# Performance work log

Hardware: AMD Instinct MI355X
Metric: run time of the kernel (lower is better)

## Reference

```python
import jax, jax.numpy as jnp
import numpy as np

N_BITS = 3        # routing dims (slice_mask = first 3 indices)
N_HEADS = 8       # 2**N_BITS
D_FEAT = 512      # input_dim - N_BITS
D_BASE = 1024     # base MLP output
D_HEAD_H = 1024   # head hidden
D_OUT = 512       # head output
BATCH = 8192


def setup_inputs() -> dict:
    key = jax.random.key(0)
    ks = jax.random.split(key, 8)
    s = lambda fan_in: 1.0 / np.sqrt(fan_in)
    x = jax.random.normal(ks[0], (BATCH, N_BITS + D_FEAT), dtype=jnp.float32)
    Wb = jax.random.normal(ks[1], (D_FEAT, D_BASE), dtype=jnp.float32) * s(D_FEAT)
    bb = jax.random.normal(ks[2], (D_BASE,), dtype=jnp.float32) * s(D_FEAT)
    Wh1 = jax.random.normal(ks[3], (N_HEADS, D_BASE, D_HEAD_H), dtype=jnp.float32) * s(D_BASE)
    bh1 = jax.random.normal(ks[4], (N_HEADS, D_HEAD_H), dtype=jnp.float32) * s(D_BASE)
    Wh2 = jax.random.normal(ks[5], (N_HEADS, D_HEAD_H, D_OUT), dtype=jnp.float32) * s(D_HEAD_H)
    bh2 = jax.random.normal(ks[6], (N_HEADS, D_OUT), dtype=jnp.float32) * s(D_HEAD_H)
    return {"x": x, "Wb": Wb, "bb": bb, "Wh1": Wh1, "bh1": bh1, "Wh2": Wh2, "bh2": bh2}


def _combs():
    # Faithful to the torch `recursive` construction for three single-index
    # binary slices: combs[bit, head] = (head >> bit) & 1
    return ((jnp.arange(N_HEADS)[None, :] >> jnp.arange(N_BITS)[:, None]) & 1).astype(bool)


def reference(x, Wb, bb, Wh1, bh1, Wh2, bh2):
    bits = x[:, :N_BITS] > 0.5          # [B, 3] routing bits
    feat = x[:, N_BITS:]                # [B, 512]
    base = jax.nn.relu(feat @ Wb + bb)  # [B, 1024] shared base net
    # all heads run over the full batch (as in the original module)
    h = jax.nn.relu(jnp.einsum('bd,hde->bhe', base, Wh1) + bh1[None])  # [B, 8, 1024]
    out_all = jnp.einsum('bhe,heo->bho', h, Wh2) + bh2[None]           # [B, 8, 512]
    combs = _combs()                                                   # [3, 8]
    sel = jnp.all(bits[:, :, None] == combs[None], axis=1).astype(x.dtype)  # [B, 8] one-hot
    return jnp.einsum('bho,bh->bo', out_all, sel)                      # [B, 512]
```

## Files before the change

kernel.cpp:

```cpp
#include <hip/hip_runtime.h>
#include <hip/hip_bf16.h>
#include <stdint.h>

using short8 = __attribute__((ext_vector_type(8))) short;
using f32x4  = __attribute__((ext_vector_type(4))) float;

#define NBITS 3
#define NHEADS 8
#define BATCH 8192
#define DFEAT 512
#define DBASE 1024
#define DHH   1024
#define DOUT  512
#define XCOLS (NBITS + DFEAT)

static __device__ __forceinline__ unsigned short f2bf(float f) {
    union { float f; unsigned u; } v; v.f = f;
    unsigned r = v.u + 0x7FFFu + ((v.u >> 16) & 1u);
    return (unsigned short)(r >> 16);
}

__global__ void k_bucket(const float* __restrict__ x, int* __restrict__ cnt,
                         int* __restrict__ rows) {
    int r = blockIdx.x * 256 + threadIdx.x;
    if (r >= BATCH) return;
    const float* xr = x + (size_t)r * XCOLS;
    int h = (xr[0] > 0.5f ? 1 : 0) | (xr[1] > 0.5f ? 2 : 0) | (xr[2] > 0.5f ? 4 : 0);
    int slot = atomicAdd(cnt + h, 1);
    rows[h * BATCH + slot] = r;
}

__global__ void k_feat(const float* __restrict__ x, unsigned short* __restrict__ feat) {
    int t = blockIdx.x * 256 + threadIdx.x;
    int row = t >> 6, c8 = (t & 63) << 3;
    const float* src = x + (size_t)row * XCOLS + NBITS + c8;
    short8 v;
#pragma unroll
    for (int i = 0; i < 8; ++i) v[i] = (short)f2bf(src[i]);
    *(short8*)(feat + (size_t)row * DFEAT + c8) = v;
}

__global__ void k_transpose(const float* __restrict__ W, unsigned short* __restrict__ WT,
                            int K, int N) {
    __shared__ float tile[32][33];
    int b  = blockIdx.z;
    int n0 = blockIdx.x << 5, k0 = blockIdx.y << 5;
    int tx = threadIdx.x & 31, ty = threadIdx.x >> 5;
    const float* Wb = W + (size_t)b * K * N;
    unsigned short* WTb = WT + (size_t)b * K * N;
#pragma unroll
    for (int j = 0; j < 32; j += 8)
        tile[ty + j][tx] = Wb[(size_t)(k0 + ty + j) * N + n0 + tx];
    __syncthreads();
#pragma unroll
    for (int j = 0; j < 32; j += 8)
        WTb[(size_t)(n0 + ty + j) * K + k0 + tx] = f2bf(tile[tx][ty + j]);
}

template<bool GATHER, bool RELU, bool OUTBF16>
__global__ __launch_bounds__(256, 2)
void k_gemm(const unsigned short* __restrict__ A, int lda, int K,
            const unsigned short* __restrict__ BT,
            const float* __restrict__ bias,
            void* __restrict__ C, int ldc,
            const int* __restrict__ rowsAll, const int* __restrict__ cntAll,
            int Nfull) {
    const int head = blockIdx.z;
    const int m0 = blockIdx.x * 128;
    const int n0 = blockIdx.y * 128;
    int M = BATCH;
    const int* rows = nullptr;
    if (GATHER) {
        M = cntAll[head];
        if (m0 >= M) return;
        rows = rowsAll + head * BATCH;
    }
    const unsigned short* BTh = BT + (size_t)head * Nfull * K;
    const float* biash = bias + (size_t)head * Nfull;

    __shared__ __align__(16) unsigned short As[128 * 32];
    __shared__ __align__(16) unsigned short Bs[128 * 32];

    const int t    = threadIdx.x;
    const int wave = t >> 6;
    const int lane = t & 63;
    const int wr = wave >> 1, wc = wave & 1;

    const unsigned short* gA[2];
    const unsigned short* gB[2];
#pragma unroll
    for (int p = 0; p < 2; ++p) {
        int i = p * 256 + t;
        int idx = m0 + (i >> 2);
        int r;
        if (GATHER) { if (idx >= M) idx = M - 1; r = rows[idx]; }
        else r = idx;
        gA[p] = A + (size_t)r * lda + (i & 3) * 8;
        int nrow = n0 + (i >> 2);
        gB[p] = BTh + (size_t)nrow * K + (i & 3) * 8;
    }
    char* lAs = (char*)As;
    char* lBs = (char*)Bs;

    f32x4 acc[4][4] = {};
    const int ln = lane & 15, lq = lane >> 4;

    for (int kt = 0; kt < K; kt += 32) {
#pragma unroll
        for (int p = 0; p < 2; ++p) {
            __builtin_amdgcn_global_load_lds(
                (const __attribute__((address_space(1))) void*)(gA[p] + kt),
                (__attribute__((address_space(3))) void*)(lAs + (p * 256 + wave * 64) * 16),
                16, 0, 0);
            __builtin_amdgcn_global_load_lds(
                (const __attribute__((address_space(1))) void*)(gB[p] + kt),
                (__attribute__((address_space(3))) void*)(lBs + (p * 256 + wave * 64) * 16),
                16, 0, 0);
        }
        __syncthreads();
        short8 af[4], bfr[4];
#pragma unroll
        for (int m = 0; m < 4; ++m)
            af[m] = *(const short8*)(As + (wr * 64 + m * 16 + ln) * 32 + lq * 8);
#pragma unroll
        for (int n = 0; n < 4; ++n)
            bfr[n] = *(const short8*)(Bs + (wc * 64 + n * 16 + ln) * 32 + lq * 8);
#pragma unroll
        for (int m = 0; m < 4; ++m)
#pragma unroll
            for (int n = 0; n < 4; ++n)
                acc[m][n] = __builtin_amdgcn_mfma_f32_16x16x32_bf16(af[m], bfr[n], acc[m][n], 0, 0, 0);
        __syncthreads();
    }

#pragma unroll
    for (int n = 0; n < 4; ++n) {
        int col = n0 + wc * 64 + n * 16 + ln;
        float bv = biash[col];
#pragma unroll
        for (int m = 0; m < 4; ++m) {
#pragma unroll
            for (int r = 0; r < 4; ++r) {
                int lr = wr * 64 + m * 16 + lq * 4 + r;
                int grow;
                if (GATHER) {
                    if (m0 + lr >= M) continue;
                    grow = rows[m0 + lr];
                } else {
                    grow = m0 + lr;
                }
                float v = acc[m][n][r] + bv;
                if (RELU) v = fmaxf(v, 0.0f);
                if (OUTBF16)
                    ((unsigned short*)C)[(size_t)grow * ldc + col] = f2bf(v);
                else
                    ((float*)C)[(size_t)grow * ldc + col] = v;
            }
        }
    }
}

extern "C" void kernel_launch(void* const* d_in, const int* in_sizes, int n_in,
                              void* d_out, int out_size, void* d_ws, size_t ws_size,
                              hipStream_t stream) {
    const float* x   = (const float*)d_in[0];
    const float* Wb  = (const float*)d_in[1];
    const float* bb  = (const float*)d_in[2];
    const float* Wh1 = (const float*)d_in[3];
    const float* bh1 = (const float*)d_in[4];
    const float* Wh2 = (const float*)d_in[5];
    const float* bh2 = (const float*)d_in[6];

    char* ws = (char*)d_ws;
    unsigned short* feat = (unsigned short*)(ws);
    unsigned short* WbT  = (unsigned short*)(ws + (8ull  << 20));
    unsigned short* Wh1T = (unsigned short*)(ws + (9ull  << 20));
    unsigned short* Wh2T = (unsigned short*)(ws + (25ull << 20));
    unsigned short* base = (unsigned short*)(ws + (33ull << 20));
    unsigned short* hbuf = (unsigned short*)(ws + (49ull << 20));
    int* rows            = (int*)(ws + (65ull << 20));
    int* cnt             = (int*)(ws + (65ull << 20) + (256ull << 10));

    hipMemsetAsync(cnt, 0, NHEADS * sizeof(int), stream);
    k_bucket<<<BATCH / 256, 256, 0, stream>>>(x, cnt, rows);
    k_feat<<<(BATCH * 64) / 256, 256, 0, stream>>>(x, feat);
    k_transpose<<<dim3(DBASE / 32, DFEAT / 32, 1), 256, 0, stream>>>(Wb, WbT, DFEAT, DBASE);
    k_transpose<<<dim3(DHH / 32, DBASE / 32, NHEADS), 256, 0, stream>>>(Wh1, Wh1T, DBASE, DHH);
    k_transpose<<<dim3(DOUT / 32, DHH / 32, NHEADS), 256, 0, stream>>>(Wh2, Wh2T, DHH, DOUT);

    k_gemm<false, true, true><<<dim3(64, DBASE / 128, 1), 256, 0, stream>>>(
        feat, DFEAT, DFEAT, WbT, bb, base, DBASE, nullptr, nullptr, DBASE);
    k_gemm<true, true, true><<<dim3(64, DHH / 128, NHEADS), 256, 0, stream>>>(
        base, DBASE, DBASE, Wh1T, bh1, hbuf, DHH, rows, cnt, DHH);
    k_gemm<true, false, false><<<dim3(64, DOUT / 128, NHEADS), 256, 0, stream>>>(
        hbuf, DHH, DHH, Wh2T, bh2, d_out, DOUT, rows, cnt, DOUT);
}
```

Baseline: 328.7 us.

## Double-buffer LDS tiles in GEMM to overlap global loads with MFMA

```diff
diff --git a/kernel.cpp b/kernel.cpp
--- a/kernel.cpp
+++ b/kernel.cpp
@@ -78,8 +78,8 @@
     const unsigned short* BTh = BT + (size_t)head * Nfull * K;
     const float* biash = bias + (size_t)head * Nfull;
 
-    __shared__ __align__(16) unsigned short As[128 * 32];
-    __shared__ __align__(16) unsigned short Bs[128 * 32];
+    __shared__ __align__(16) unsigned short As[2][128 * 32];
+    __shared__ __align__(16) unsigned short Bs[2][128 * 32];
 
     const int t    = threadIdx.x;
     const int wave = t >> 6;
@@ -101,37 +101,50 @@
     }
     char* lAs = (char*)As;
     char* lBs = (char*)Bs;
+    const int dstOff = (wave * 64) * 16;
+
+#define STAGE(koff, buf)                                                              \
+    {                                                                                 \
+        _Pragma("unroll")                                                             \
+        for (int p = 0; p < 2; ++p) {                                                 \
+            __builtin_amdgcn_global_load_lds(                                         \
+                (const __attribute__((address_space(1))) void*)(gA[p] + (koff)),      \
+                (__attribute__((address_space(3))) void*)(lAs + (buf) * 8192 + p * 4096 + dstOff), \
+                16, 0, 0);                                                            \
+            __builtin_amdgcn_global_load_lds(                                         \
+                (const __attribute__((address_space(1))) void*)(gB[p] + (koff)),      \
+                (__attribute__((address_space(3))) void*)(lBs + (buf) * 8192 + p * 4096 + dstOff), \
+                16, 0, 0);                                                            \
+        }                                                                             \
+    }
 
     f32x4 acc[4][4] = {};
     const int ln = lane & 15, lq = lane >> 4;
-
-    for (int kt = 0; kt < K; kt += 32) {
-#pragma unroll
-        for (int p = 0; p < 2; ++p) {
-            __builtin_amdgcn_global_load_lds(
-                (const __attribute__((address_space(1))) void*)(gA[p] + kt),
-                (__attribute__((address_space(3))) void*)(lAs + (p * 256 + wave * 64) * 16),
-                16, 0, 0);
-            __builtin_amdgcn_global_load_lds(
-                (const __attribute__((address_space(1))) void*)(gB[p] + kt),
-                (__attribute__((address_space(3))) void*)(lBs + (p * 256 + wave * 64) * 16),
-                16, 0, 0);
-        }
-        __syncthreads();
+    const int nt = K >> 5;
+
+    STAGE(0, 0);
+    __syncthreads();
+
+    for (int tk = 0; tk < nt; ++tk) {
+        const int cur = tk & 1;
+        if (tk + 1 < nt) STAGE((tk + 1) << 5, cur ^ 1);
+
         short8 af[4], bfr[4];
 #pragma unroll
         for (int m = 0; m < 4; ++m)
-            af[m] = *(const short8*)(As + (wr * 64 + m * 16 + ln) * 32 + lq * 8);
+            af[m] = *(const short8*)(As[cur] + (wr * 64 + m * 16 + ln) * 32 + lq * 8);
 #pragma unroll
         for (int n = 0; n < 4; ++n)
-            bfr[n] = *(const short8*)(Bs + (wc * 64 + n * 16 + ln) * 32 + lq * 8);
+            bfr[n] = *(const short8*)(Bs[cur] + (wc * 64 + n * 16 + ln) * 32 + lq * 8);
 #pragma unroll
         for (int m = 0; m < 4; ++m)
 #pragma unroll
             for (int n = 0; n < 4; ++n)
                 acc[m][n] = __builtin_amdgcn_mfma_f32_16x16x32_bf16(af[m], bfr[n], acc[m][n], 0, 0, 0);
+
         __syncthreads();
     }
+#undef STAGE
 
 #pragma unroll
     for (int n = 0; n < 4; ++n) {
```

Result: no change. 327.0 us (-0.5%).

## Rewrite GEMM with 128x256 tiles, double-buffered swizzled LDS and software pipelining

Applied to the files above, without the earlier changes.

```diff
diff --git a/kernel.cpp b/kernel.cpp
--- a/kernel.cpp
+++ b/kernel.cpp
@@ -58,16 +58,19 @@
 }
 
 template<bool GATHER, bool RELU, bool OUTBF16>
-__global__ __launch_bounds__(256, 2)
-void k_gemm(const unsigned short* __restrict__ A, int lda, int K,
-            const unsigned short* __restrict__ BT,
-            const float* __restrict__ bias,
-            void* __restrict__ C, int ldc,
-            const int* __restrict__ rowsAll, const int* __restrict__ cntAll,
-            int Nfull) {
-    const int head = blockIdx.z;
-    const int m0 = blockIdx.x * 128;
-    const int n0 = blockIdx.y * 128;
+__global__ __launch_bounds__(512, 1)
+void k_gemm2(const unsigned short* __restrict__ A, int lda, int K,
+             const unsigned short* __restrict__ BT,
+             const float* __restrict__ bias,
+             void* __restrict__ C, int ldc,
+             const int* __restrict__ rowsAll, const int* __restrict__ cntAll,
+             int Nfull, int nshift) {
+    const int bid  = blockIdx.x;
+    const int mt   = bid & 63;
+    const int nt   = (bid >> 6) & ((1 << nshift) - 1);
+    const int head = GATHER ? (bid >> (6 + nshift)) : 0;
+    const int m0 = mt * 128;
+    const int n0 = nt * 256;
     int M = BATCH;
     const int* rows = nullptr;
     if (GATHER) {
@@ -78,60 +81,95 @@
     const unsigned short* BTh = BT + (size_t)head * Nfull * K;
     const float* biash = bias + (size_t)head * Nfull;
 
-    __shared__ __align__(16) unsigned short As[128 * 32];
-    __shared__ __align__(16) unsigned short Bs[128 * 32];
+    __shared__ __align__(16) char lds[98304];
+    char* ldsp = lds;
 
     const int t    = threadIdx.x;
-    const int wave = t >> 6;
+    const int w    = t >> 6;
     const int lane = t & 63;
-    const int wr = wave >> 1, wc = wave & 1;
+    const int wr = w >> 2, wc = w & 3;
+    const int ln = lane & 15, lq = lane >> 4;
 
     const unsigned short* gA[2];
-    const unsigned short* gB[2];
-#pragma unroll
-    for (int p = 0; p < 2; ++p) {
-        int i = p * 256 + t;
-        int idx = m0 + (i >> 2);
-        int r;
-        if (GATHER) { if (idx >= M) idx = M - 1; r = rows[idx]; }
-        else r = idx;
-        gA[p] = A + (size_t)r * lda + (i & 3) * 8;
-        int nrow = n0 + (i >> 2);
-        gB[p] = BTh + (size_t)nrow * K + (i & 3) * 8;
-    }
-    char* lAs = (char*)As;
-    char* lBs = (char*)Bs;
+    {
+        int rl  = t >> 3;
+        int kch = (t & 7) ^ (rl & 7);
+#pragma unroll
+        for (int h = 0; h < 2; ++h) {
+            int idx = m0 + h * 64 + rl;
+            int r;
+            if (GATHER) { idx = idx < M ? idx : (M - 1); r = rows[idx]; }
+            else r = idx;
+            gA[h] = A + (size_t)r * lda + kch * 8;
+        }
+    }
+    const unsigned short* gB[2][2];
+#pragma unroll
+    for (int hb = 0; hb < 2; ++hb)
+#pragma unroll
+        for (int i = 0; i < 2; ++i) {
+            int c   = i * 512 + t;
+            int cl  = c >> 3;
+            int kch = (c & 7) ^ (cl & 7);
+            int ncol = n0 + hb * 128 + cl;
+            gB[hb][i] = BTh + (size_t)ncol * K + kch * 8;
+        }
+
+#define STAGE_A(kt, d)                                                                     \
+    { _Pragma("unroll") for (int h = 0; h < 2; ++h)                                        \
+        __builtin_amdgcn_global_load_lds(                                                  \
+            (const __attribute__((address_space(1))) void*)(gA[h] + (kt) * 64),            \
+            (__attribute__((address_space(3))) void*)(ldsp + (d) * 16384 + h * 8192 + w * 1024), \
+            16, 0, 0); }
+#define STAGE_B(kt, d)                                                                     \
+    { _Pragma("unroll") for (int hb = 0; hb < 2; ++hb)                                     \
+      _Pragma("unroll") for (int i = 0; i < 2; ++i)                                        \
+        __builtin_amdgcn_global_load_lds(                                                  \
+            (const __attribute__((address_space(1))) void*)(gB[hb][i] + (kt) * 64),        \
+            (__attribute__((address_space(3))) void*)(ldsp + 32768 + (d) * 32768 + hb * 16384 + i * 8192 + w * 1024), \
+            16, 0, 0); }
+#define LOAD_A(dst, d, ks)                                                                 \
+    { _Pragma("unroll") for (int m = 0; m < 4; ++m) {                                      \
+        int rA = wr * 64 + m * 16 + ln;                                                    \
+        int ch = (((ks) << 2) | lq) ^ (ln & 7);                                            \
+        dst[m] = *(const short8*)(ldsp + (d) * 16384 + rA * 128 + ch * 16); } }
+#define LOAD_B(dst, d, ks)                                                                 \
+    { _Pragma("unroll") for (int n = 0; n < 4; ++n) {                                      \
+        int cB = wc * 64 + n * 16 + ln;                                                    \
+        int ch = (((ks) << 2) | lq) ^ (ln & 7);                                            \
+        dst[n] = *(const short8*)(ldsp + 32768 + (d) * 32768 + cB * 128 + ch * 16); } }
+#define MFMA16(av, bv)                                                                     \
+    { __builtin_amdgcn_s_setprio(1);                                                       \
+      _Pragma("unroll") for (int m = 0; m < 4; ++m)                                        \
+      _Pragma("unroll") for (int n = 0; n < 4; ++n)                                        \
+        acc[m][n] = __builtin_amdgcn_mfma_f32_16x16x32_bf16(av[m], bv[n], acc[m][n], 0, 0, 0); \
+      __builtin_amdgcn_s_setprio(0); }
 
     f32x4 acc[4][4] = {};
-    const int ln = lane & 15, lq = lane >> 4;
-
-    for (int kt = 0; kt < K; kt += 32) {
-#pragma unroll
-        for (int p = 0; p < 2; ++p) {
-            __builtin_amdgcn_global_load_lds(
-                (const __attribute__((address_space(1))) void*)(gA[p] + kt),
-                (__attribute__((address_space(3))) void*)(lAs + (p * 256 + wave * 64) * 16),
-                16, 0, 0);
-            __builtin_amdgcn_global_load_lds(
-                (const __attribute__((address_space(1))) void*)(gB[p] + kt),
-                (__attribute__((address_space(3))) void*)(lBs + (p * 256 + wave * 64) * 16),
-                16, 0, 0);
-        }
+    short8 a0[4], b0[4], a1[4], b1[4];
+    const int NT = K >> 6;
+
+    STAGE_A(0, 0); STAGE_B(0, 0); STAGE_A(1, 1);
+    __syncthreads();
+    LOAD_A(a0, 0, 0); LOAD_B(b0, 0, 0);
+
+    for (int kt = 0; kt < NT; ++kt) {
+        const int d = kt & 1, o = d ^ 1;
+        const int kB = (kt + 1 < NT) ? kt + 1 : NT - 1;
+        const int kA = (kt + 2 < NT) ? kt + 2 : NT - 1;
+        STAGE_B(kB, o);
+        LOAD_A(a1, d, 1); LOAD_B(b1, d, 1);
+        MFMA16(a0, b0);
         __syncthreads();
-        short8 af[4], bfr[4];
-#pragma unroll
-        for (int m = 0; m < 4; ++m)
-            af[m] = *(const short8*)(As + (wr * 64 + m * 16 + ln) * 32 + lq * 8);
-#pragma unroll
-        for (int n = 0; n < 4; ++n)
-            bfr[n] = *(const short8*)(Bs + (wc * 64 + n * 16 + ln) * 32 + lq * 8);
-#pragma unroll
-        for (int m = 0; m < 4; ++m)
-#pragma unroll
-            for (int n = 0; n < 4; ++n)
-                acc[m][n] = __builtin_amdgcn_mfma_f32_16x16x32_bf16(af[m], bfr[n], acc[m][n], 0, 0, 0);
-        __syncthreads();
-    }
+        STAGE_A(kA, d);
+        LOAD_A(a0, o, 0); LOAD_B(b0, o, 0);
+        MFMA16(a1, b1);
+    }
+#undef STAGE_A
+#undef STAGE_B
+#undef LOAD_A
+#undef LOAD_B
+#undef MFMA16
 
 #pragma unroll
     for (int n = 0; n < 4; ++n) {
@@ -140,16 +178,16 @@
 #pragma unroll
         for (int m = 0; m < 4; ++m) {
 #pragma unroll
-            for (int r = 0; r < 4; ++r) {
-                int lr = wr * 64 + m * 16 + lq * 4 + r;
+            for (int j = 0; j < 4; ++j) {
+                int rt = wr * 64 + m * 16 + lq * 4 + j;
                 int grow;
                 if (GATHER) {
-                    if (m0 + lr >= M) continue;
-                    grow = rows[m0 + lr];
+                    if (m0 + rt >= M) continue;
+                    grow = rows[m0 + rt];
                 } else {
-                    grow = m0 + lr;
+                    grow = m0 + rt;
                 }
-                float v = acc[m][n][r] + bv;
+                float v = acc[m][n][j] + bv;
                 if (RELU) v = fmaxf(v, 0.0f);
                 if (OUTBF16)
                     ((unsigned short*)C)[(size_t)grow * ldc + col] = f2bf(v);
@@ -188,10 +226,10 @@
     k_transpose<<<dim3(DHH / 32, DBASE / 32, NHEADS), 256, 0, stream>>>(Wh1, Wh1T, DBASE, DHH);
     k_transpose<<<dim3(DOUT / 32, DHH / 32, NHEADS), 256, 0, stream>>>(Wh2, Wh2T, DHH, DOUT);
 
-    k_gemm<false, true, true><<<dim3(64, DBASE / 128, 1), 256, 0, stream>>>(
-        feat, DFEAT, DFEAT, WbT, bb, base, DBASE, nullptr, nullptr, DBASE);
-    k_gemm<true, true, true><<<dim3(64, DHH / 128, NHEADS), 256, 0, stream>>>(
-        base, DBASE, DBASE, Wh1T, bh1, hbuf, DHH, rows, cnt, DHH);
-    k_gemm<true, false, false><<<dim3(64, DOUT / 128, NHEADS), 256, 0, stream>>>(
-        hbuf, DHH, DHH, Wh2T, bh2, d_out, DOUT, rows, cnt, DOUT);
-}
+    k_gemm2<false, true, true><<<256, 512, 0, stream>>>(
+        feat, DFEAT, DFEAT, WbT, bb, base, DBASE, nullptr, nullptr, DBASE, 2);
+    k_gemm2<true, true, true><<<2048, 512, 0, stream>>>(
+        base, DBASE, DBASE, Wh1T, bh1, hbuf, DHH, rows, cnt, DHH, 2);
+    k_gemm2<true, false, false><<<1024, 512, 0, stream>>>(
+        hbuf, DHH, DHH, Wh2T, bh2, d_out, DOUT, rows, cnt, DOUT, 1);
+}
```

Measured after the change: 323.9 us. Within noise of the previous version (-1.5%).
